# Optimization experiments

Measured on AMD Instinct MI355X. Metric: run time of the kernel, lower is better.

The kernel has to match this reference:

```python
import jax, jax.numpy as jnp
import numpy as np

B, T, N, M, P, YD = 256, 64, 128, 256, 256, 1


def lstm_cell(x, h, c, Wih, Whh, bih, bhh):
    # torch LSTM gate order: i, f, g, o
    gates = x @ Wih.T + h @ Whh.T + bih + bhh  # (B, 4H)
    i, f, g, o = jnp.split(gates, 4, axis=-1)
    c_new = jax.nn.sigmoid(f) * c + jax.nn.sigmoid(i) * jnp.tanh(g)
    h_new = jax.nn.sigmoid(o) * jnp.tanh(c_new)
    return h_new, c_new


def setup_inputs() -> dict:
    key = jax.random.key(0)
    ks = jax.random.split(key, 20)
    s = 0.05
    return {
        "inputs": jax.random.normal(ks[0], (B, T, N + YD), jnp.float32),
        "WU_e": jax.random.normal(ks[1], (T, 2 * M + T), jnp.float32) * s,
        "v_e": jax.random.normal(ks[2], (1, T), jnp.float32) * s,
        "Wih_e": jax.random.normal(ks[3], (4 * M, N), jnp.float32) * s,
        "Whh_e": jax.random.normal(ks[4], (4 * M, M), jnp.float32) * s,
        "bih_e": jax.random.normal(ks[5], (4 * M,), jnp.float32) * s,
        "bhh_e": jax.random.normal(ks[6], (4 * M,), jnp.float32) * s,
        "WU_d": jax.random.normal(ks[7], (M, 2 * P + M), jnp.float32) * s,
        "v_d": jax.random.normal(ks[8], (1, M), jnp.float32) * s,
        "wb_tilde": jax.random.normal(ks[9], (1, YD + M), jnp.float32) * s,
        "Wih_d": jax.random.normal(ks[10], (4 * P, 1), jnp.float32) * s,
        "Whh_d": jax.random.normal(ks[11], (4 * P, P), jnp.float32) * s,
        "bih_d": jax.random.normal(ks[12], (4 * P,), jnp.float32) * s,
        "bhh_d": jax.random.normal(ks[13], (4 * P,), jnp.float32) * s,
        "Wb_W": jax.random.normal(ks[14], (P, P + M), jnp.float32) * s,
        "Wb_b": jax.random.normal(ks[15], (P,), jnp.float32) * s,
        "vb_W": jax.random.normal(ks[16], (YD, P), jnp.float32) * s,
        "vb_b": jax.random.normal(ks[17], (YD,), jnp.float32) * s,
    }


def _darnn(inputs, WU_e, v_e, Wih_e, Whh_e, bih_e, bhh_e,
           WU_d, v_d, wb_tilde, Wih_d, Whh_d, bih_d, bhh_d,
           Wb_W, Wb_b, vb_W, vb_b):
    X = inputs[:, :, :N]          # (B, T, N)
    Y = inputs[:, :, N:]          # (B, T, YD)
    X_nt = jnp.transpose(X, (0, 2, 1))  # (B, N, T), constant across encoder steps

    # ---------------- Encoder ----------------
    def enc_step(carry, x_t):  # x_t: (B, N)
        h, c = carry
        hs = jnp.concatenate([h, c], axis=-1)  # (B, 2M)
        feat = jnp.concatenate(
            [jnp.broadcast_to(hs[:, None, :], (B, N, 2 * M)), X_nt], axis=-1)  # (B, N, 2M+T)
        E = (jnp.tanh(feat @ WU_e.T) @ v_e.T)[..., 0]  # (B, N)
        alpha = jax.nn.softmax(E, axis=1)
        h, c = lstm_cell(x_t * alpha, h, c, Wih_e, Whh_e, bih_e, bhh_e)
        return (h, c), h

    h0 = jnp.zeros((B, M), inputs.dtype)
    c0 = jnp.zeros((B, M), inputs.dtype)
    _, X_encoded = jax.lax.scan(enc_step, (h0, c0), jnp.transpose(X, (1, 0, 2)))
    Xe_bm = jnp.transpose(X_encoded, (1, 0, 2))  # (B, T, M)

    # ---------------- Decoder ----------------
    def dec_step(carry, y_t):  # y_t: (B, YD)
        h, c, _ = carry
        hs = jnp.concatenate([h, c], axis=-1)  # (B, 2P)
        feat = jnp.concatenate(
            [jnp.broadcast_to(hs[:, None, :], (B, T, 2 * P)), Xe_bm], axis=-1)  # (B, T, 2P+M)
        l = (jnp.tanh(feat @ WU_d.T) @ v_d.T)[..., 0]  # (B, T)
        beta = jax.nn.softmax(l, axis=1)
        ctx = jnp.einsum('bt,btm->bm', beta, Xe_bm)  # (B, M)
        y_tilde = jnp.concatenate([y_t, ctx], axis=-1) @ wb_tilde.T  # (B, 1)
        h, c = lstm_cell(y_tilde, h, c, Wih_d, Whh_d, bih_d, bhh_d)
        return (h, c, ctx), None

    hd0 = jnp.zeros((B, P), inputs.dtype)
    cd0 = jnp.zeros((B, P), inputs.dtype)
    ctx0 = jnp.zeros((B, M), inputs.dtype)
    (h, c, ctx), _ = jax.lax.scan(
        dec_step, (hd0, cd0, ctx0), jnp.transpose(Y[:, :T - 1, :], (1, 0, 2)))

    hidden = jnp.concatenate([h, ctx], axis=-1) @ Wb_W.T + Wb_b  # (B, P)
    y_hat = hidden @ vb_W.T + vb_b  # (B, YD)
    return y_hat


def reference(inputs, WU_e, v_e, Wih_e, Whh_e, bih_e, bhh_e,
              WU_d, v_d, wb_tilde, Wih_d, Whh_d, bih_d, bhh_d,
              Wb_W, Wb_b, vb_W, vb_b):
    return _darnn(inputs, WU_e, v_e, Wih_e, Whh_e, bih_e, bhh_e,
                  WU_d, v_d, wb_tilde, Wih_d, Whh_d, bih_d, bhh_d,
                  Wb_W, Wb_b, vb_W, vb_b)
```

## Files before the change

kernel.cpp:

```cpp
#include <hip/hip_runtime.h>
#include <math.h>


#define OFF_XWT   0u
#define OFF_XEWT  2097152u
#define OFF_XE    6291456u
#define OFF_HE    10485760u
#define OFF_HD    10616832u
#define OFF_SB    10747904u
#define OFF_SDB   10780672u
#define OFF_XA    10911744u
#define OFF_CTX   10944512u
#define OFF_YT    11010048u
#define OFF_BAR   11010304u
#define WS_END    11010816u

#define SLAB_F 24576
#define PER_F  2432
#define SCR_F  12288
#define FLG_F  16
#define SMEM_F (SLAB_F + PER_F + SCR_F + FLG_F)
#define SMEM_BYTES (SMEM_F * 4)

#define F_E 0
#define F_L 1
#define F_B 2
#define F_Y 3

__device__ __forceinline__ float fast_tanh(float x) {
  float xc = fminf(15.f, fmaxf(-15.f, x));
  float e = __expf(2.f * xc);
  return 1.f - 2.f * __builtin_amdgcn_rcpf(e + 1.f);
}
__device__ __forceinline__ float fast_sig(float x) {
  float xc = fminf(30.f, fmaxf(-30.f, x));
  return __builtin_amdgcn_rcpf(1.f + __expf(-xc));
}
__device__ __forceinline__ float wave_max(float v) {
#pragma unroll
  for (int o = 32; o; o >>= 1) v = fmaxf(v, __shfl_xor(v, o));
  return v;
}
__device__ __forceinline__ float wave_sum(float v) {
#pragma unroll
  for (int o = 32; o; o >>= 1) v += __shfl_xor(v, o);
  return v;
}
__device__ __forceinline__ float dot4(float4 a, float4 b) {
  return a.x*b.x + a.y*b.y + a.z*b.z + a.w*b.w;
}

__device__ __forceinline__ void st1_sc1(float* p, float v) {
  asm volatile("global_store_dword %0, %1, off sc1" :: "v"(p), "v"(v) : "memory");
}
__device__ __forceinline__ void ld1q_sc1(float4& a, const float* pa) {
  asm volatile("global_load_dwordx4 %0, %1, off sc1\n\ts_waitcnt vmcnt(0)"
               : "=&v"(a) : "v"(pa) : "memory");
}
__device__ __forceinline__ void ld1q_nw(float4& a, const float* pa) {
  asm volatile("global_load_dwordx4 %0, %1, off sc1"
               : "=&v"(a) : "v"(pa) : "memory");
}
__device__ __forceinline__ void vm0() {
  asm volatile("s_waitcnt vmcnt(0)" ::: "memory");
}
__device__ __forceinline__ void lgk0() {
  asm volatile("s_waitcnt lgkmcnt(0)" ::: "memory");
}
__device__ __forceinline__ float ld1s_sc1(const float* p) {
  float v;
  asm volatile("global_load_dword %0, %1, off sc1\n\ts_waitcnt vmcnt(0)"
               : "=&v"(v) : "v"(p) : "memory");
  return v;
}
__device__ __forceinline__ void ld8s_sc1(
    float& a0,float& a1,float& a2,float& a3,float& a4,float& a5,float& a6,float& a7,
    const float* p0,const float* p1,const float* p2,const float* p3,
    const float* p4,const float* p5,const float* p6,const float* p7) {
  asm volatile(
      "global_load_dword %0, %8, off sc1\n\t"
      "global_load_dword %1, %9, off sc1\n\t"
      "global_load_dword %2, %10, off sc1\n\t"
      "global_load_dword %3, %11, off sc1\n\t"
      "global_load_dword %4, %12, off sc1\n\t"
      "global_load_dword %5, %13, off sc1\n\t"
      "global_load_dword %6, %14, off sc1\n\t"
      "global_load_dword %7, %15, off sc1\n\t"
      "s_waitcnt vmcnt(0)"
      : "=&v"(a0),"=&v"(a1),"=&v"(a2),"=&v"(a3),
        "=&v"(a4),"=&v"(a5),"=&v"(a6),"=&v"(a7)
      : "v"(p0),"v"(p1),"v"(p2),"v"(p3),"v"(p4),"v"(p5),"v"(p6),"v"(p7)
      : "memory");
}
__device__ __forceinline__ void atomic_add_sc1(float* p, float v) {
  asm volatile("global_atomic_add_f32 %0, %1, off sc1" :: "v"(p), "v"(v) : "memory");
}

__device__ __forceinline__ void lds_inc(unsigned* f) {
  __hip_atomic_fetch_add(f, 1u, __ATOMIC_RELAXED, __HIP_MEMORY_SCOPE_WORKGROUP);
}
__device__ __forceinline__ void lds_poll(unsigned* f, unsigned tgt) {
  unsigned cur;
  do { cur = __hip_atomic_load(f, __ATOMIC_RELAXED, __HIP_MEMORY_SCOPE_WORKGROUP); } while (cur < tgt);
  asm volatile("" ::: "memory");
}

#define FMA16V(a0,a1,a2,a3,xv,wv) \
  a0.x += xv.x*wv.x; a0.y += xv.x*wv.y; a0.z += xv.x*wv.z; a0.w += xv.x*wv.w; \
  a1.x += xv.y*wv.x; a1.y += xv.y*wv.y; a1.z += xv.y*wv.z; a1.w += xv.y*wv.w; \
  a2.x += xv.z*wv.x; a2.y += xv.z*wv.y; a2.z += xv.z*wv.z; a2.w += xv.z*wv.w; \
  a3.x += xv.w*wv.x; a3.y += xv.w*wv.y; a3.z += xv.w*wv.z; a3.w += xv.w*wv.w;

__device__ __forceinline__ void bar_arrive(unsigned* bar) {
  asm volatile("s_waitcnt vmcnt(0)" ::: "memory");
  __syncthreads();
  if (threadIdx.x == 0)
    __hip_atomic_fetch_add(bar, 1u, __ATOMIC_RELAXED, __HIP_MEMORY_SCOPE_AGENT);
}
__device__ __forceinline__ void bar_wait(unsigned* bar, unsigned target) {
  if (threadIdx.x == 0) {
    unsigned cur;
    do {
      __builtin_amdgcn_s_sleep(1);
      cur = __hip_atomic_load(bar, __ATOMIC_RELAXED, __HIP_MEMORY_SCOPE_AGENT);
    } while (cur < target);
  }
  __syncthreads();
}

__global__ void darnn_init(float* __restrict__ ws, float* __restrict__ out) {
  unsigned i = blockIdx.x * 256u + threadIdx.x;
  const unsigned span = WS_END - OFF_HE;
  for (unsigned idx = i; idx < span; idx += gridDim.x * 256u) ws[OFF_HE + idx] = 0.f;
  if (i < 256u) out[i] = 0.f;
}

__global__ __launch_bounds__(512, 2) void darnn_main(
    const float* __restrict__ in,   const float* __restrict__ WUe,   const float* __restrict__ ve,
    const float* __restrict__ Wih_e,const float* __restrict__ Whh_e,
    const float* __restrict__ bih_e,const float* __restrict__ bhh_e,
    const float* __restrict__ WUd,  const float* __restrict__ vd,
    const float* __restrict__ wbt,  const float* __restrict__ Wih_d,
    const float* __restrict__ Whh_d,const float* __restrict__ bih_d, const float* __restrict__ bhh_d,
    const float* __restrict__ WbW,  const float* __restrict__ Wbb,
    const float* __restrict__ vbW,  const float* __restrict__ vbb,
    float* __restrict__ ws, float* __restrict__ out)
{
  extern __shared__ __align__(16) float sm[];
  float* SLAB = sm;
  float* PER  = sm + SLAB_F;
  float* SCR  = sm + SLAB_F + PER_F;
  unsigned* FLG = (unsigned*)(sm + SLAB_F + PER_F + SCR_F);
  const int tid = threadIdx.x;
  const int bid = blockIdx.x;
  const int grp = bid >> 4;
  const int mt  = bid & 15;
  const int b0  = grp << 4;

  float* XWt  = ws + OFF_XWT;
  float* XeWt = ws + OFF_XEWT;
  float* Xe   = ws + OFF_XE;
  unsigned* barp = (unsigned*)(ws + OFF_BAR) + grp * 32;
  unsigned barn = 0;

  if (tid < FLG_F) FLG[tid] = 0u;

  float* wue_s  = PER;
  float* ve_s   = PER + 2304;
  float* bsum_e = PER + 2368;

  const int jfixE = ((tid & 63) + mt * 4) & 63;

  {
    int r = tid & 63, kq = tid >> 6;
    int grow = (r & 3) * 256 + mt * 16 + (r >> 2);
#pragma unroll 4
    for (int q = 0; q < 12; ++q) {
      int k = kq * 48 + q * 4;
      float4 wv = (k < 128) ? *(const float4*)(Wih_e + grow * 128 + k)
                            : *(const float4*)(Whh_e + grow * 256 + (k - 128));
      SLAB[(k + 0) * 64 + r] = wv.x; SLAB[(k + 1) * 64 + r] = wv.y;
      SLAB[(k + 2) * 64 + r] = wv.z; SLAB[(k + 3) * 64 + r] = wv.w;
    }
    {
      int lin = tid * 4;
      int j = lin >> 5, c0 = lin & 31;
      int col = (c0 < 16) ? (mt * 16 + c0) : (256 + mt * 16 + (c0 - 16));
      float4 wv = *(const float4*)(WUe + j * 576 + col);
      *(float4*)(wue_s + j * 36 + c0) = wv;
    }
    if (tid < 64) {
      ve_s[tid] = ve[tid];
      int g = tid >> 4, m2 = tid & 15, m = mt * 16 + m2;
      bsum_e[tid] = bih_e[g * 256 + m] + bhh_e[g * 256 + m];
    }
  }

  {
    float* Xs = SCR;
    const float* Xb = in + bid * 8256;
    __syncthreads();
    for (int it = 0; it < 16; ++it) {
      int lin = tid + it * 512;
      int k = lin >> 7, n = lin & 127;
      Xs[n * 68 + k] = Xb[k * 129 + n];
    }
    __syncthreads();
    int j = tid & 63, nh = tid >> 6;
    float acc[16];
#pragma unroll
    for (int i = 0; i < 16; ++i) acc[i] = 0.f;
    const float* wrow = WUe + j * 576 + 512;
    for (int kc = 0; kc < 4; ++kc) {
      float4 w0 = *(const float4*)(wrow + kc * 16 + 0);
      float4 w1 = *(const float4*)(wrow + kc * 16 + 4);
      float4 w2 = *(const float4*)(wrow + kc * 16 + 8);
      float4 w3 = *(const float4*)(wrow + kc * 16 + 12);
#pragma unroll
      for (int ni = 0; ni < 16; ++ni) {
        const float* xp = Xs + (nh * 16 + ni) * 68 + kc * 16;
        acc[ni] += dot4(*(const float4*)(xp + 0),  w0) + dot4(*(const float4*)(xp + 4),  w1)
                 + dot4(*(const float4*)(xp + 8),  w2) + dot4(*(const float4*)(xp + 12), w3);
      }
    }
    float* dst = XWt + bid * 8192 + j * 128 + nh * 16;
#pragma unroll
    for (int ni = 0; ni < 16; ++ni) dst[ni] = acc[ni];
    __syncthreads();
  }

  float4 whc[8];
#pragma unroll
  for (int q = 0; q < 8; ++q) whc[q] = *(const float4*)(wue_s + jfixE * 36 + q * 4);
  float4 bsE = {0,0,0,0};
  {
    int m2 = tid & 15;
    bsE.x = bsum_e[m2]; bsE.y = bsum_e[16 + m2];
    bsE.z = bsum_e[32 + m2]; bsE.w = bsum_e[48 + m2];
  }
  float xwreg[32];
  if (tid < 256) {
    int w = tid >> 6, l = tid & 63;
    const float* xwp = XWt + bid * 8192;
#pragma unroll
    for (int jj = 0; jj < 16; ++jj) {
      xwreg[jj]      = xwp[(w * 16 + jj) * 128 + l];
      xwreg[16 + jj] = xwp[(w * 16 + jj) * 128 + 64 + l];
    }
  }
  float c_reg = 0.f;

  for (int t = 0; t < 64; ++t) {
    const int rd = t & 1, wr2 = (t + 1) & 1;
    float* xah = SCR + 1024;
    const int ks = tid >> 6, ml = (tid >> 2) & 15, b4 = tid & 3;
    float4 a0 = {0,0,0,0}, a1 = {0,0,0,0}, a2 = {0,0,0,0}, a3 = {0,0,0,0};

    bar_wait(barp, barn);

    if (tid < 256) {
      int w = tid >> 6, l = tid & 63;
      float* Sj = SCR;
      float* Ep = SCR + 64;
      if (l < 16)
        Sj[w * 16 + l] = ld1s_sc1(ws + OFF_SB + (unsigned)rd * 16384 + (unsigned)bid * 64 + w * 16 + l);
      lgk0();
      float e0 = 0.f, e1 = 0.f;
#pragma unroll
      for (int jj = 0; jj < 16; ++jj) {
        float s = Sj[w * 16 + jj];
        float vv = ve_s[w * 16 + jj];
        e0 += vv * fast_tanh(xwreg[jj] + s);
        e1 += vv * fast_tanh(xwreg[16 + jj] + s);
      }
      Ep[w * 128 + l] = e0;
      Ep[w * 128 + 64 + l] = e1;
      lgk0();
      if (l == 0) lds_inc(FLG + F_E);
      if (w == 0) {
        lds_poll(FLG + F_E, 4u * (t + 1));
        float En0 = Ep[l] + Ep[128 + l] + Ep[256 + l] + Ep[384 + l];
        float En1 = Ep[64 + l] + Ep[192 + l] + Ep[320 + l] + Ep[448 + l];
        float mx = wave_max(fmaxf(En0, En1));
        float ex0 = __expf(En0 - mx), ex1 = __expf(En1 - mx);
        float tot = wave_sum(ex0 + ex1);
        float rt = __builtin_amdgcn_rcpf(tot);
        float x0 = in[bid * 8256 + t * 129 + l];
        float x1 = in[bid * 8256 + t * 129 + 64 + l];
        float* XAg = ws + OFF_XA + (unsigned)grp * 2048;
        st1_sc1(XAg + l * 16 + mt, x0 * ex0 * rt);
        st1_sc1(XAg + (64 + l) * 16 + mt, x1 * ex1 * rt);
        vm0();
        if (tid == 0)
          __hip_atomic_fetch_add(barp, 1u, __ATOMIC_RELAXED, __HIP_MEMORY_SCOPE_AGENT);
      }
    } else {
      int u = tid - 256;
      float4 h0, h1, h2, h3;
      const float* hb = ws + OFF_HE + (unsigned)rd * 65536 + (unsigned)grp * 4096 + u * 16;
      ld1q_nw(h0, hb); ld1q_nw(h1, hb + 4); ld1q_nw(h2, hb + 8); ld1q_nw(h3, hb + 12);
      vm0();
      float* row = xah + (unsigned)(128 + u) * 20;
      *(float4*)(row + 0) = h0; *(float4*)(row + 4) = h1;
      *(float4*)(row + 8) = h2; *(float4*)(row + 12) = h3;
      lgk0();
      int s = u >> 6;
      const float* xp = xah + (unsigned)(128 + s * 64) * 20 + b4 * 4;
      const float* wp = SLAB + (unsigned)(128 + s * 64) * 64 + ml * 4;
#pragma unroll 8
      for (int kk = 0; kk < 64; ++kk) {
        float4 xv = *(const float4*)(xp + kk * 20);
        float4 wv = *(const float4*)(wp + kk * 64);
        FMA16V(a0, a1, a2, a3, xv, wv);
      }
    }
    barn += 16;
    bar_wait(barp, barn);

    if (tid < 16) {
      float* sp = ws + OFF_SB + (unsigned)rd * 16384 + (unsigned)bid * 64 + tid * 4;
      st1_sc1(sp + 0, 0.f); st1_sc1(sp + 1, 0.f);
      st1_sc1(sp + 2, 0.f); st1_sc1(sp + 3, 0.f);
    }
    {
      int l = tid & 63;
      int k = (ks << 4) + (l >> 2), i4 = (l & 3) * 4;
      float4 q;
      ld1q_sc1(q, ws + OFF_XA + (unsigned)grp * 2048 + k * 16 + i4);
      *(float4*)(xah + k * 20 + i4) = q;
      lgk0();
    }
    {
      const float* xp = xah + (unsigned)(ks * 16) * 20 + b4 * 4;
      const float* wp = SLAB + (unsigned)(ks * 16) * 64 + ml * 4;
#pragma unroll 8
      for (int kk = 0; kk < 16; ++kk) {
        float4 xv = *(const float4*)(xp + kk * 20);
        float4 wv = *(const float4*)(wp + kk * 64);
        FMA16V(a0, a1, a2, a3, xv, wv);
      }
    }
    __syncthreads();
    float* red = SCR;
    {
      float* rp = red + (unsigned)(ks * 64 + ml * 4 + b4) * 20;
      *(float4*)(rp + 0) = a0; *(float4*)(rp + 4) = a1;
      *(float4*)(rp + 8) = a2; *(float4*)(rp + 12) = a3;
    }
    __syncthreads();
    float* hcs = SCR + 10240;
    if (tid < 256) {
      int m2 = tid & 15, bl = tid >> 4;
      int t2 = m2 * 4 + (bl >> 2), bs = bl & 3;
      float4 gate = {0,0,0,0};
#pragma unroll
      for (int k2 = 0; k2 < 8; ++k2) {
        float4 rr = *(const float4*)(red + (unsigned)(k2 * 64 + t2) * 20 + bs * 4);
        gate.x += rr.x; gate.y += rr.y; gate.z += rr.z; gate.w += rr.w;
      }
      float gi = gate.x + bsE.x, gf = gate.y + bsE.y;
      float gg = gate.z + bsE.z, go = gate.w + bsE.w;
      float cn = fast_sig(gf) * c_reg + fast_sig(gi) * fast_tanh(gg);
      float hn = fast_sig(go) * fast_tanh(cn);
      c_reg = cn;
      unsigned m = mt * 16 + m2;
      st1_sc1(ws + OFF_HE + (unsigned)wr2 * 65536 + (unsigned)grp * 4096 + m * 16 + bl, hn);
      st1_sc1(Xe + ((unsigned)(b0 + bl) * 64 + t) * 256 + m, hn);
      hcs[bl * 32 + m2] = hn;
      hcs[bl * 32 + 16 + m2] = cn;
    }
    __syncthreads();
    {
      int wq = tid >> 6;
#pragma unroll
      for (int e2 = 0; e2 < 2; ++e2) {
        int bl2 = wq * 2 + e2;
        const float* hp = hcs + bl2 * 32;
        float s = 0.f;
#pragma unroll
        for (int q = 0; q < 4; ++q) {
          s += dot4(*(const float4*)(hp + q * 4), whc[q]);
          s += dot4(*(const float4*)(hp + 16 + q * 4), whc[4 + q]);
        }
        atomic_add_sc1(ws + OFF_SB + (unsigned)wr2 * 16384 + (unsigned)(b0 + bl2) * 64 + jfixE, s);
      }
    }
    barn += 16;
    bar_arrive(barp);
  }
  bar_wait(barp, barn);

  float xe[64];
  if (tid < 256) {
    const float* xb = Xe + (unsigned)bid * 16384 + tid;
#pragma unroll
    for (int g8 = 0; g8 < 8; ++g8) {
      ld8s_sc1(xe[g8*8+0], xe[g8*8+1], xe[g8*8+2], xe[g8*8+3],
               xe[g8*8+4], xe[g8*8+5], xe[g8*8+6], xe[g8*8+7],
               xb + (g8*8+0)*256, xb + (g8*8+1)*256, xb + (g8*8+2)*256,
               xb + (g8*8+3)*256, xb + (g8*8+4)*256, xb + (g8*8+5)*256,
               xb + (g8*8+6)*256, xb + (g8*8+7)*256);
    }
  }

  float* vd_s   = PER;
  float* wbt_s  = PER + 256;
  float* bsum_d = PER + 520;
  float* wihd_s = PER + 584;
  float* wudT   = SLAB + 16384;
  const int jfixD = ((tid & 255) + mt * 16) & 255;
  __syncthreads();
  {
    int r = tid & 63, kq = tid >> 6;
    int grow = (r & 3) * 256 + mt * 16 + (r >> 2);
#pragma unroll 4
    for (int q = 0; q < 8; ++q) {
      int k = kq * 32 + q * 4;
      float4 wv = *(const float4*)(Whh_d + grow * 256 + k);
      SLAB[(k + 0) * 64 + r] = wv.x; SLAB[(k + 1) * 64 + r] = wv.y;
      SLAB[(k + 2) * 64 + r] = wv.z; SLAB[(k + 3) * 64 + r] = wv.w;
    }
    {
      int j = tid & 255, half = tid >> 8;
#pragma unroll
      for (int i = 0; i < 16; ++i) {
        int c = half * 16 + i;
        int col = (c < 16) ? (mt * 16 + c) : (256 + mt * 16 + (c - 16));
        wudT[c * 256 + j] = WUd[(unsigned)j * 768 + col];
      }
    }
    if (tid < 256) vd_s[tid] = vd[tid];
    if (tid < 257) wbt_s[tid] = wbt[tid];
    if (tid < 64) {
      int g = tid >> 4, m2 = tid & 15, m = mt * 16 + m2;
      bsum_d[tid] = bih_d[g * 256 + m] + bhh_d[g * 256 + m];
      wihd_s[tid] = Wih_d[g * 256 + m];
    }
  }
  __syncthreads();

  {
    float* XeT = SCR;
    float* Wdc = SCR + 4096;
    int tt2 = tid & 15, jq = tid >> 4;
    for (int jc = 0; jc < 2; ++jc) {
      float4 c0 = {0,0,0,0}, c1 = {0,0,0,0}, c2 = {0,0,0,0}, c3 = {0,0,0,0};
      for (int kc = 0; kc < 4; ++kc) {
        __syncthreads();
        if (tid < 256 && (tid >> 6) == kc) {
          int kk = tid & 63;
#pragma unroll
          for (int t4 = 0; t4 < 16; ++t4) {
            float4 v = { xe[t4*4+0], xe[t4*4+1], xe[t4*4+2], xe[t4*4+3] };
            *(float4*)(XeT + kk * 64 + t4 * 4) = v;
          }
        }
        {
          int jj = tid >> 2, k16 = (tid & 3) * 16;
          const float* src = WUd + (unsigned)(jc * 128 + jj) * 768 + 512 + kc * 64 + k16;
#pragma unroll
          for (int s4 = 0; s4 < 4; ++s4) {
            float4 wv = *(const float4*)(src + s4 * 4);
            Wdc[(k16 + s4*4 + 0) * 128 + jj] = wv.x;
            Wdc[(k16 + s4*4 + 1) * 128 + jj] = wv.y;
            Wdc[(k16 + s4*4 + 2) * 128 + jj] = wv.z;
            Wdc[(k16 + s4*4 + 3) * 128 + jj] = wv.w;
          }
        }
        __syncthreads();
#pragma unroll 8
        for (int kk = 0; kk < 64; ++kk) {
          float4 xv = *(const float4*)(XeT + kk * 64 + tt2 * 4);
          float4 wv = *(const float4*)(Wdc + kk * 128 + jq * 4);
          FMA16V(c0, c1, c2, c3, wv, xv);
        }
      }
      int jb = jc * 128 + jq * 4;
      *(float4*)(XeWt + ((unsigned)bid * 256 + jb + 0) * 64 + tt2 * 4) = c0;
      *(float4*)(XeWt + ((unsigned)bid * 256 + jb + 1) * 64 + tt2 * 4) = c1;
      *(float4*)(XeWt + ((unsigned)bid * 256 + jb + 2) * 64 + tt2 * 4) = c2;
      *(float4*)(XeWt + ((unsigned)bid * 256 + jb + 3) * 64 + tt2 * 4) = c3;
    }
    __syncthreads();
  }

  float wreg[32];
#pragma unroll
  for (int c = 0; c < 32; ++c) wreg[c] = wudT[c * 256 + jfixD];
  float4 bsD = {0,0,0,0}, wiD = {0,0,0,0};
  {
    int m2 = tid & 15;
    bsD.x = bsum_d[m2]; bsD.y = bsum_d[16 + m2]; bsD.z = bsum_d[32 + m2]; bsD.w = bsum_d[48 + m2];
    wiD.x = wihd_s[m2]; wiD.y = wihd_s[16 + m2]; wiD.z = wihd_s[32 + m2]; wiD.w = wihd_s[48 + m2];
  }
  float xewreg[64];
  if (tid < 256) {
    int w = tid >> 6, l = tid & 63;
    const float* xew = XeWt + (unsigned)bid * 16384 + l;
#pragma unroll
    for (int jj = 0; jj < 64; ++jj) xewreg[jj] = xew[(w * 64 + jj) << 6];
  }
  float cd_reg = 0.f;

  for (int t = 0; t < 63; ++t) {
    const int rd = t & 1, wr2 = (t + 1) & 1;
    const int ml = (tid >> 2) & 15, b4 = tid & 3;
    float* hT  = SCR + 2048;
    float* red = SCR + 7168;

    bar_wait(barp, barn);

    if (tid < 256) {
      int w = tid >> 6, l = tid & 63;
      float* Sdj  = SCR;
      float* lp   = SCR + 256;
      float* beta = SCR + 512;
      float* r8   = SCR + 576;
      Sdj[w * 64 + l] = ld1s_sc1(ws + OFF_SDB + (unsigned)rd * 65536 + (unsigned)bid * 256 + w * 64 + l);
      lgk0();
      float lpar = 0.f;
#pragma unroll 8
      for (int jj = 0; jj < 64; ++jj)
        lpar += vd_s[w * 64 + jj] * fast_tanh(xewreg[jj] + Sdj[w * 64 + jj]);
      lp[w * 64 + l] = lpar;
      lgk0();
      if (l == 0) lds_inc(FLG + F_L);
      if (w == 0) {
        lds_poll(FLG + F_L, 4u * (t + 1));
        float lv = lp[l] + lp[64 + l] + lp[128 + l] + lp[192 + l];
        float mx = wave_max(lv);
        float ex = __expf(lv - mx);
        float sw = wave_sum(ex);
        beta[l] = ex * __builtin_amdgcn_rcpf(sw);
        lgk0();
        if (l == 0) lds_inc(FLG + F_B);
      }
      lds_poll(FLG + F_B, (unsigned)(t + 1));
      lgk0();
      float ctx = 0.f;
#pragma unroll
      for (int tt = 0; tt < 64; ++tt) ctx += beta[tt] * xe[tt];
      st1_sc1(ws + OFF_CTX + (unsigned)bid * 256 + tid, ctx);
      float yp = ctx * wbt_s[1 + tid];
      float swv = wave_sum(yp);
      if (l == 0) r8[w] = swv;
      lgk0();
      if (l == 0) lds_inc(FLG + F_Y);
      if (w == 0) {
        lds_poll(FLG + F_Y, 4u * (t + 1));
        if (l == 0) {
          float yt = wbt_s[0] * in[bid * 8256 + t * 129 + 128] + r8[0] + r8[1] + r8[2] + r8[3];
          st1_sc1(ws + OFF_YT + bid, yt);
        }
        vm0();
        if (tid == 0)
          __hip_atomic_fetch_add(barp, 1u, __ATOMIC_RELAXED, __HIP_MEMORY_SCOPE_AGENT);
      }
    } else {
      int u = tid - 256;
      float4 h0, h1, h2, h3;
      const float* hb = ws + OFF_HD + (unsigned)rd * 65536 + (unsigned)grp * 4096 + u * 16;
      ld1q_nw(h0, hb); ld1q_nw(h1, hb + 4); ld1q_nw(h2, hb + 8); ld1q_nw(h3, hb + 12);
      vm0();
      float* row = hT + (unsigned)u * 20;
      *(float4*)(row + 0) = h0; *(float4*)(row + 4) = h1;
      *(float4*)(row + 8) = h2; *(float4*)(row + 12) = h3;
      lgk0();
      int s = u >> 6;
      float4 a0 = {0,0,0,0}, a1 = {0,0,0,0}, a2 = {0,0,0,0}, a3 = {0,0,0,0};
      const float* xp = hT + (unsigned)(s * 64) * 20 + b4 * 4;
      const float* wp = SLAB + (unsigned)(s * 64) * 64 + ml * 4;
#pragma unroll 8
      for (int kk = 0; kk < 64; ++kk) {
        float4 xv = *(const float4*)(xp + kk * 20);
        float4 wv = *(const float4*)(wp + kk * 64);
        FMA16V(a0, a1, a2, a3, xv, wv);
      }
      float* rp = red + (unsigned)(s * 64 + ml * 4 + b4) * 20;
      *(float4*)(rp + 0) = a0; *(float4*)(rp + 4) = a1;
      *(float4*)(rp + 8) = a2; *(float4*)(rp + 12) = a3;
    }
    barn += 16;
    __syncthreads();

    float4 gate = {0,0,0,0};
    if (tid < 256) {
      int m2 = tid & 15, bl = tid >> 4;
      int t2 = m2 * 4 + (bl >> 2), bs = bl & 3;
#pragma unroll
      for (int k2 = 0; k2 < 4; ++k2) {
        float4 rr = *(const float4*)(red + (unsigned)(k2 * 64 + t2) * 20 + bs * 4);
        gate.x += rr.x; gate.y += rr.y; gate.z += rr.z; gate.w += rr.w;
      }
    }
    bar_wait(barp, barn);
    if (tid < 64) {
      float* sp = ws + OFF_SDB + (unsigned)rd * 65536 + (unsigned)bid * 256 + tid * 4;
      st1_sc1(sp + 0, 0.f); st1_sc1(sp + 1, 0.f);
      st1_sc1(sp + 2, 0.f); st1_sc1(sp + 3, 0.f);
    }
    float* hcs = SCR;
    if (tid < 256) {
      int m2 = tid & 15, bl = tid >> 4;
      float yt_reg = ld1s_sc1(ws + OFF_YT + b0 + bl);
      float gi = gate.x + yt_reg * wiD.x + bsD.x;
      float gf = gate.y + yt_reg * wiD.y + bsD.y;
      float gg = gate.z + yt_reg * wiD.z + bsD.z;
      float go = gate.w + yt_reg * wiD.w + bsD.w;
      float cn = fast_sig(gf) * cd_reg + fast_sig(gi) * fast_tanh(gg);
      float hn = fast_sig(go) * fast_tanh(cn);
      cd_reg = cn;
      unsigned m = mt * 16 + m2;
      st1_sc1(ws + OFF_HD + (unsigned)wr2 * 65536 + (unsigned)grp * 4096 + m * 16 + bl, hn);
      hcs[bl * 32 + m2] = hn;
      hcs[bl * 32 + 16 + m2] = cn;
    }
    __syncthreads();
    {
      int half = tid >> 8;
#pragma unroll
      for (int e2 = 0; e2 < 8; ++e2) {
        int bl2 = half * 8 + e2;
        const float* hp = hcs + bl2 * 32;
        float s = 0.f;
#pragma unroll
        for (int c = 0; c < 16; ++c) s += hp[c] * wreg[c];
#pragma unroll
        for (int c = 0; c < 16; ++c) s += hp[16 + c] * wreg[16 + c];
        atomic_add_sc1(ws + OFF_SDB + (unsigned)wr2 * 65536 + (unsigned)(b0 + bl2) * 256 + jfixD, s);
      }
    }
    barn += 16;
    bar_arrive(barp);
  }
  bar_wait(barp, barn);

  {
    float* hsf  = SCR;
    float* hid2 = SCR + 8256;
    {
      int l0 = tid * 2, l1 = tid * 2 + 1;
      int k0 = l0 >> 2, i0 = l0 & 3, k1 = l1 >> 2, i1 = l1 & 3;
      const float* hb = ws + OFF_HD + 65536u + (unsigned)grp * 4096;
      int bl0 = l0 >> 6, c0 = (l0 & 63) * 4, bl1 = l1 >> 6, c1 = (l1 & 63) * 4;
      float4 qa, qb, qc, qd;
      ld1q_nw(qa, hb + k0 * 16 + i0 * 4);
      ld1q_nw(qb, hb + k1 * 16 + i1 * 4);
      ld1q_nw(qc, ws + OFF_CTX + (unsigned)(b0 + bl0) * 256 + c0);
      ld1q_nw(qd, ws + OFF_CTX + (unsigned)(b0 + bl1) * 256 + c1);
      vm0();
      hsf[(i0 * 4 + 0) * 516 + k0] = qa.x; hsf[(i0 * 4 + 1) * 516 + k0] = qa.y;
      hsf[(i0 * 4 + 2) * 516 + k0] = qa.z; hsf[(i0 * 4 + 3) * 516 + k0] = qa.w;
      hsf[(i1 * 4 + 0) * 516 + k1] = qb.x; hsf[(i1 * 4 + 1) * 516 + k1] = qb.y;
      hsf[(i1 * 4 + 2) * 516 + k1] = qb.z; hsf[(i1 * 4 + 3) * 516 + k1] = qb.w;
      *(float4*)(hsf + bl0 * 516 + 256 + c0) = qc;
      *(float4*)(hsf + bl1 * 516 + 256 + c1) = qd;
    }
    __syncthreads();
    int bl = tid & 15, p4 = (tid >> 4) & 15, half = tid >> 8;
    int row = mt * 16 + p4;
    const float* wrow = WbW + (unsigned)row * 512 + half * 256;
    const float* hp = hsf + bl * 516 + half * 256;
    float acc = half ? 0.f : Wbb[row];
#pragma unroll 8
    for (int q = 0; q < 64; ++q)
      acc += dot4(*(const float4*)(hp + q * 4), *(const float4*)(wrow + q * 4));
    hid2[half * 272 + bl * 17 + p4] = acc;
    __syncthreads();
    if (tid < 16) {
      float s = 0.f;
#pragma unroll
      for (int p = 0; p < 16; ++p)
        s += (hid2[tid * 17 + p] + hid2[272 + tid * 17 + p]) * vbW[mt * 16 + p];
      if (mt == 0) s += vbb[0];
      atomicAdd(&out[b0 + tid], s);
    }
  }
}

extern "C" void kernel_launch(void* const* d_in, const int* in_sizes, int n_in,
                              void* d_out, int out_size, void* d_ws, size_t ws_size,
                              hipStream_t stream) {
  (void)in_sizes; (void)n_in; (void)out_size; (void)ws_size;
  const float* in    = (const float*)d_in[0];
  const float* WUe   = (const float*)d_in[1];
  const float* ve    = (const float*)d_in[2];
  const float* Wih_e = (const float*)d_in[3];
  const float* Whh_e = (const float*)d_in[4];
  const float* bih_e = (const float*)d_in[5];
  const float* bhh_e = (const float*)d_in[6];
  const float* WUd   = (const float*)d_in[7];
  const float* vd    = (const float*)d_in[8];
  const float* wbt   = (const float*)d_in[9];
  const float* Wih_d = (const float*)d_in[10];
  const float* Whh_d = (const float*)d_in[11];
  const float* bih_d = (const float*)d_in[12];
  const float* bhh_d = (const float*)d_in[13];
  const float* WbW   = (const float*)d_in[14];
  const float* Wbb   = (const float*)d_in[15];
  const float* vbW   = (const float*)d_in[16];
  const float* vbb   = (const float*)d_in[17];
  float* ws  = (float*)d_ws;
  float* out = (float*)d_out;

  (void)hipFuncSetAttribute((const void*)darnn_main,
                            hipFuncAttributeMaxDynamicSharedMemorySize, SMEM_BYTES);
  hipLaunchKernelGGL(darnn_init, dim3(1024), dim3(256), 0, stream, ws, out);
  hipLaunchKernelGGL(darnn_main, dim3(256), dim3(512), SMEM_BYTES, stream,
                     in, WUe, ve, Wih_e, Whh_e, bih_e, bhh_e,
                     WUd, vd, wbt, Wih_d, Whh_d, bih_d, bhh_d,
                     WbW, Wbb, vbW, vbb, ws, out);
}
```

Baseline: 1.330 ms.

## Replace group barriers with per-value sentinel flags for attention and y_tilde exchange

Removes two 16-block atomic barrier round-trips per timestep in the encoder and decoder. Consumers now spin on the data itself: slots are pre-filled with a NaN sentinel and polled until the real value appears. The attention vector moves into the unused XEWT region with double-buffered slots, and y_tilde into a spare SB area. This shortens the cross-block critical path but relies on single-word store visibility ordering and on sentinel resets being placed correctly, and it adds per-thread polling traffic.

```diff
diff --git a/kernel.cpp b/kernel.cpp
--- a/kernel.cpp
+++ b/kernel.cpp
@@ -15,6 +15,8 @@
 #define OFF_BAR   11010304u
 #define WS_END    11010816u
 
+#define SENT_U 0x7FC00001u
+
 #define SLAB_F 24576
 #define PER_F  2432
 #define SCR_F  12288
@@ -72,6 +74,10 @@
   asm volatile("global_load_dword %0, %1, off sc1\n\ts_waitcnt vmcnt(0)"
                : "=&v"(v) : "v"(p) : "memory");
   return v;
+}
+__device__ __forceinline__ bool sent4(const float4& q) {
+  return __float_as_uint(q.x) == SENT_U || __float_as_uint(q.y) == SENT_U ||
+         __float_as_uint(q.z) == SENT_U || __float_as_uint(q.w) == SENT_U;
 }
 __device__ __forceinline__ void ld8s_sc1(
     float& a0,float& a1,float& a2,float& a3,float& a4,float& a5,float& a6,float& a7,
@@ -118,20 +124,23 @@
     __hip_atomic_fetch_add(bar, 1u, __ATOMIC_RELAXED, __HIP_MEMORY_SCOPE_AGENT);
 }
 __device__ __forceinline__ void bar_wait(unsigned* bar, unsigned target) {
-  if (threadIdx.x == 0) {
-    unsigned cur;
-    do {
-      __builtin_amdgcn_s_sleep(1);
-      cur = __hip_atomic_load(bar, __ATOMIC_RELAXED, __HIP_MEMORY_SCOPE_AGENT);
-    } while (cur < target);
-  }
-  __syncthreads();
+  unsigned cur = __hip_atomic_load(bar, __ATOMIC_RELAXED, __HIP_MEMORY_SCOPE_AGENT);
+  while (cur < target) {
+    __builtin_amdgcn_s_sleep(1);
+    cur = __hip_atomic_load(bar, __ATOMIC_RELAXED, __HIP_MEMORY_SCOPE_AGENT);
+  }
+  asm volatile("" ::: "memory");
 }
 
 __global__ void darnn_init(float* __restrict__ ws, float* __restrict__ out) {
   unsigned i = blockIdx.x * 256u + threadIdx.x;
   const unsigned span = WS_END - OFF_HE;
   for (unsigned idx = i; idx < span; idx += gridDim.x * 256u) ws[OFF_HE + idx] = 0.f;
+  unsigned* wsu = (unsigned*)ws;
+  for (unsigned idx = i; idx < 65536u; idx += gridDim.x * 256u) {
+    unsigned g = idx >> 12, off = idx & 4095u;
+    wsu[OFF_XEWT + g * 262144u + off] = SENT_U;
+  }
   if (i < 256u) out[i] = 0.f;
 }
 
@@ -156,6 +165,7 @@
   const int grp = bid >> 4;
   const int mt  = bid & 15;
   const int b0  = grp << 4;
+  const float SENTF = __uint_as_float(SENT_U);
 
   float* XWt  = ws + OFF_XWT;
   float* XeWt = ws + OFF_XEWT;
@@ -287,15 +297,17 @@
         float rt = __builtin_amdgcn_rcpf(tot);
         float x0 = in[bid * 8256 + t * 129 + l];
         float x1 = in[bid * 8256 + t * 129 + 64 + l];
-        float* XAg = ws + OFF_XA + (unsigned)grp * 2048;
+        float* XAg = ws + OFF_XEWT + (unsigned)grp * 262144u + (unsigned)rd * 2048u;
         st1_sc1(XAg + l * 16 + mt, x0 * ex0 * rt);
         st1_sc1(XAg + (64 + l) * 16 + mt, x1 * ex1 * rt);
-        vm0();
-        if (tid == 0)
-          __hip_atomic_fetch_add(barp, 1u, __ATOMIC_RELAXED, __HIP_MEMORY_SCOPE_AGENT);
       }
     } else {
       int u = tid - 256;
+      if (u < 64) {
+        float* XAr = ws + OFF_XEWT + (unsigned)grp * 262144u + (unsigned)wr2 * 2048u;
+        st1_sc1(XAr + u * 16 + mt, SENTF);
+        st1_sc1(XAr + (64 + u) * 16 + mt, SENTF);
+      }
       float4 h0, h1, h2, h3;
       const float* hb = ws + OFF_HE + (unsigned)rd * 65536 + (unsigned)grp * 4096 + u * 16;
       ld1q_nw(h0, hb); ld1q_nw(h1, hb + 4); ld1q_nw(h2, hb + 8); ld1q_nw(h3, hb + 12);
@@ -314,19 +326,20 @@
         FMA16V(a0, a1, a2, a3, xv, wv);
       }
     }
-    barn += 16;
-    bar_wait(barp, barn);
 
     if (tid < 16) {
       float* sp = ws + OFF_SB + (unsigned)rd * 16384 + (unsigned)bid * 64 + tid * 4;
-      st1_sc1(sp + 0, 0.f); st1_sc1(sp + 1, 0.f);
+      float z01 = (t == 63 && tid == 0) ? SENTF : 0.f;
+      st1_sc1(sp + 0, z01); st1_sc1(sp + 1, z01);
       st1_sc1(sp + 2, 0.f); st1_sc1(sp + 3, 0.f);
     }
     {
       int l = tid & 63;
       int k = (ks << 4) + (l >> 2), i4 = (l & 3) * 4;
+      const float* src = ws + OFF_XEWT + (unsigned)grp * 262144u + (unsigned)rd * 2048u + k * 16 + i4;
       float4 q;
-      ld1q_sc1(q, ws + OFF_XA + (unsigned)grp * 2048 + k * 16 + i4);
+      ld1q_sc1(q, src);
+      while (sent4(q)) { __builtin_amdgcn_s_sleep(1); ld1q_sc1(q, src); }
       *(float4*)(xah + k * 20 + i4) = q;
       lgk0();
     }
@@ -550,13 +563,12 @@
         lds_poll(FLG + F_Y, 4u * (t + 1));
         if (l == 0) {
           float yt = wbt_s[0] * in[bid * 8256 + t * 129 + 128] + r8[0] + r8[1] + r8[2] + r8[3];
-          st1_sc1(ws + OFF_YT + bid, yt);
+          st1_sc1(ws + OFF_SB + 16384u + (unsigned)bid * 64u + (unsigned)rd, yt);
         }
-        vm0();
-        if (tid == 0)
-          __hip_atomic_fetch_add(barp, 1u, __ATOMIC_RELAXED, __HIP_MEMORY_SCOPE_AGENT);
       }
     } else {
+      if (tid == 256)
+        st1_sc1(ws + OFF_SB + 16384u + (unsigned)bid * 64u + (unsigned)wr2, SENTF);
       int u = tid - 256;
       float4 h0, h1, h2, h3;
       const float* hb = ws + OFF_HD + (unsigned)rd * 65536 + (unsigned)grp * 4096 + u * 16;
@@ -580,29 +592,29 @@
       *(float4*)(rp + 0) = a0; *(float4*)(rp + 4) = a1;
       *(float4*)(rp + 8) = a2; *(float4*)(rp + 12) = a3;
     }
-    barn += 16;
-    __syncthreads();
-
-    float4 gate = {0,0,0,0};
-    if (tid < 256) {
-      int m2 = tid & 15, bl = tid >> 4;
-      int t2 = m2 * 4 + (bl >> 2), bs = bl & 3;
-#pragma unroll
-      for (int k2 = 0; k2 < 4; ++k2) {
-        float4 rr = *(const float4*)(red + (unsigned)(k2 * 64 + t2) * 20 + bs * 4);
-        gate.x += rr.x; gate.y += rr.y; gate.z += rr.z; gate.w += rr.w;
-      }
-    }
-    bar_wait(barp, barn);
     if (tid < 64) {
       float* sp = ws + OFF_SDB + (unsigned)rd * 65536 + (unsigned)bid * 256 + tid * 4;
       st1_sc1(sp + 0, 0.f); st1_sc1(sp + 1, 0.f);
       st1_sc1(sp + 2, 0.f); st1_sc1(sp + 3, 0.f);
     }
+    __syncthreads();
+
     float* hcs = SCR;
     if (tid < 256) {
       int m2 = tid & 15, bl = tid >> 4;
-      float yt_reg = ld1s_sc1(ws + OFF_YT + b0 + bl);
+      int t2 = m2 * 4 + (bl >> 2), bs = bl & 3;
+      float4 gate = {0,0,0,0};
+#pragma unroll
+      for (int k2 = 0; k2 < 4; ++k2) {
+        float4 rr = *(const float4*)(red + (unsigned)(k2 * 64 + t2) * 20 + bs * 4);
+        gate.x += rr.x; gate.y += rr.y; gate.z += rr.z; gate.w += rr.w;
+      }
+      const float* pyt = ws + OFF_SB + 16384u + (unsigned)(b0 + bl) * 64u + (unsigned)rd;
+      float yt_reg = ld1s_sc1(pyt);
+      while (__float_as_uint(yt_reg) == SENT_U) {
+        __builtin_amdgcn_s_sleep(1);
+        yt_reg = ld1s_sc1(pyt);
+      }
       float gi = gate.x + yt_reg * wiD.x + bsD.x;
       float gf = gate.y + yt_reg * wiD.y + bsD.y;
       float gg = gate.z + yt_reg * wiD.z + bsD.z;
```

After: 1.531 ms. 15.1% more time.
